# Kernel optimization log

Hardware: AMD Instinct MI355X
Metric: run time of the kernel (lower is better)

## Reference

```python
import jax, jax.numpy as jnp
import numpy as np

HIDDEN = 4096
NUM_HEADS = 32
NUM_KV_HEADS = 8
HEAD_DIM = 128


def setup_inputs() -> dict:
    key = jax.random.key(0)
    k0, k1, k2, k3, k4 = jax.random.split(key, 5)
    B, S = 1, 2048
    s = 0.02
    return {
        "hidden_states": jax.random.normal(k0, (B, S, HIDDEN), dtype=jnp.float32),
        "Wq": jax.random.normal(k1, (HIDDEN, NUM_HEADS * HEAD_DIM), dtype=jnp.float32) * s,
        "Wk": jax.random.normal(k2, (HIDDEN, NUM_KV_HEADS * HEAD_DIM), dtype=jnp.float32) * s,
        "Wv": jax.random.normal(k3, (HIDDEN, NUM_KV_HEADS * HEAD_DIM), dtype=jnp.float32) * s,
        "Wo": jax.random.normal(k4, (NUM_HEADS * HEAD_DIM, HIDDEN), dtype=jnp.float32) * s,
    }


def reference(hidden_states, Wq, Wk, Wv, Wo):
    B, S, _ = hidden_states.shape
    n_rep = NUM_HEADS // NUM_KV_HEADS
    # Projections -> [B, H, S, D]
    q = (hidden_states @ Wq).reshape(B, S, NUM_HEADS, HEAD_DIM).transpose(0, 2, 1, 3)
    k = (hidden_states @ Wk).reshape(B, S, NUM_KV_HEADS, HEAD_DIM).transpose(0, 2, 1, 3)
    v = (hidden_states @ Wv).reshape(B, S, NUM_KV_HEADS, HEAD_DIM).transpose(0, 2, 1, 3)
    # GQA expansion: repeat_interleave KV heads to match query head count
    k = jnp.repeat(k, n_rep, axis=1)
    v = jnp.repeat(v, n_rep, axis=1)
    scale = HEAD_DIM ** -0.5
    # Full [B, H, S, S] attention scores (faithful to the naive reference)
    scores = jnp.einsum("bhqd,bhkd->bhqk", q, k) * scale
    causal = jnp.tril(jnp.ones((S, S), dtype=bool))
    scores = jnp.where(causal[None, None], scores, jnp.float32(-jnp.inf))
    probs = jax.nn.softmax(scores, axis=-1)
    out = jnp.einsum("bhqk,bhkd->bhqd", probs, v)
    out = out.transpose(0, 2, 1, 3).reshape(B, S, NUM_HEADS * HEAD_DIM)
    return out @ Wo
```

## Files before the change

### kernel.cpp

```cpp
#include <hip/hip_runtime.h>
#include <hip/hip_bf16.h>

typedef __bf16 bf16;
typedef __bf16 bf16x4 __attribute__((ext_vector_type(4)));
typedef __bf16 bf16x8 __attribute__((ext_vector_type(8)));
typedef float  f32x4  __attribute__((ext_vector_type(4)));

#define SEQ  2048
#define HID  4096
#define QKVN 6144

__device__ __forceinline__ void gload_lds16(const void* g, void* l) {
  __builtin_amdgcn_global_load_lds(
      (const __attribute__((address_space(1))) void*)g,
      (__attribute__((address_space(3))) void*)l, 16, 0, 0);
}

__global__ __launch_bounds__(256) void cast_f32_bf16(const float* __restrict__ in,
                                                     bf16* __restrict__ out, int n) {
  int i = (blockIdx.x * 256 + threadIdx.x) * 4;
  int stride = gridDim.x * 256 * 4;
  for (; i < n; i += stride) {
    float4 v = *(const float4*)(in + i);
    bf16x4 o;
    o[0] = (bf16)v.x; o[1] = (bf16)v.y; o[2] = (bf16)v.z; o[3] = (bf16)v.w;
    *(bf16x4*)(out + i) = o;
  }
}

__global__ __launch_bounds__(256) void transpose_cast(const float* __restrict__ W,
                                                      bf16* __restrict__ Wt,
                                                      int N, int roff) {
  __shared__ float tile[32][33];
  int k0 = blockIdx.y * 32;
  int n0 = blockIdx.x * 32;
  int t = threadIdx.x;
  int r = t >> 5, c = t & 31;
#pragma unroll
  for (int p = 0; p < 4; ++p)
    tile[r + p * 8][c] = W[(size_t)(k0 + r + p * 8) * N + n0 + c];
  __syncthreads();
#pragma unroll
  for (int p = 0; p < 4; ++p)
    Wt[(size_t)(roff + n0 + r + p * 8) * 4096 + k0 + c] = (bf16)tile[c][r + p * 8];
}

__global__ __launch_bounds__(256) void transpose_v(const bf16* __restrict__ QKV,
                                                   bf16* __restrict__ Vt_g) {
  __shared__ bf16 tile[32][33];
  int s0 = blockIdx.x * 32;
  int d0 = blockIdx.y * 32;
  int g  = blockIdx.z;
  int t = threadIdx.x;
  int r = t >> 5, c = t & 31;
#pragma unroll
  for (int p = 0; p < 4; ++p)
    tile[r + p * 8][c] = QKV[(size_t)(s0 + r + p * 8) * QKVN + 5120 + g * 128 + d0 + c];
  __syncthreads();
#pragma unroll
  for (int p = 0; p < 4; ++p)
    Vt_g[(size_t)(g * 128 + d0 + r + p * 8) * SEQ + s0 + c] = tile[c][r + p * 8];
}

template <typename OUT_T>
__global__ __launch_bounds__(256) void gemm_bt(const bf16* __restrict__ A,
                                               const bf16* __restrict__ Bt,
                                               OUT_T* __restrict__ C,
                                               int K, int ldc) {
  __shared__ __align__(16) bf16 Abuf[128 * 64];
  __shared__ __align__(16) bf16 Bbuf[128 * 64];
  int m0 = blockIdx.y * 128, n0 = blockIdx.x * 128;
  int tid = threadIdx.x, w = tid >> 6, lane = tid & 63;
  int wr = w >> 1, wc = w & 1;
  int l15 = lane & 15, l4 = lane >> 4;
  f32x4 acc[4][4] = {};
  const int nk = K >> 6;
  for (int kt = 0; kt < nk; ++kt) {
    int k0 = kt << 6;
#pragma unroll
    for (int p = 0; p < 4; ++p) {
      int c = p * 256 + tid;
      int row = c >> 3, slot = c & 7;
      int ssl = (slot ^ (row & 7)) << 4;
      gload_lds16((const char*)(A + (size_t)(m0 + row) * K + k0) + ssl, (char*)Abuf + c * 16);
      gload_lds16((const char*)(Bt + (size_t)(n0 + row) * K + k0) + ssl, (char*)Bbuf + c * 16);
    }
    __syncthreads();
    bf16x8 af[4][2], bfr[4][2];
#pragma unroll
    for (int m = 0; m < 4; ++m)
#pragma unroll
      for (int kk = 0; kk < 2; ++kk) {
        int row = wr * 64 + m * 16 + l15;
        af[m][kk] = *(const bf16x8*)((const char*)Abuf + row * 128 +
                                     (((kk * 4 + l4) ^ (row & 7)) << 4));
      }
#pragma unroll
    for (int n = 0; n < 4; ++n)
#pragma unroll
      for (int kk = 0; kk < 2; ++kk) {
        int row = wc * 64 + n * 16 + l15;
        bfr[n][kk] = *(const bf16x8*)((const char*)Bbuf + row * 128 +
                                      (((kk * 4 + l4) ^ (row & 7)) << 4));
      }
#pragma unroll
    for (int kk = 0; kk < 2; ++kk)
#pragma unroll
      for (int m = 0; m < 4; ++m)
#pragma unroll
        for (int n = 0; n < 4; ++n)
          acc[m][n] = __builtin_amdgcn_mfma_f32_16x16x32_bf16(af[m][kk], bfr[n][kk],
                                                              acc[m][n], 0, 0, 0);
    __syncthreads();
  }
#pragma unroll
  for (int m = 0; m < 4; ++m)
#pragma unroll
    for (int n = 0; n < 4; ++n)
#pragma unroll
      for (int i = 0; i < 4; ++i) {
        int row = m0 + wr * 64 + m * 16 + l4 * 4 + i;
        int col = n0 + wc * 64 + n * 16 + l15;
        C[(size_t)row * ldc + col] = (OUT_T)acc[m][n][i];
      }
}

__global__ __launch_bounds__(512, 2) void attn_kernel(const bf16* __restrict__ QKV,
                                                      const bf16* __restrict__ Vt_g,
                                                      bf16* __restrict__ attn) {
  __shared__ __align__(16) bf16 Klds[2][64 * 128];
  __shared__ __align__(16) bf16 Vlds[2][64 * 128];
  __shared__ __align__(16) bf16 Plds[8 * 16 * 64];
  const int bid = blockIdx.x;
  const int g = bid & 7;
  const int rest = bid >> 3;
  const int hg = rest & 1;
  const int pair = rest >> 1;
  const int qb_a = pair, qb_b = 31 - pair;
  const int tid = threadIdx.x, w = tid >> 6, lane = tid & 63;
  const int hsel = w >> 2, qw = w & 3;
  const int h = g * 4 + hg * 2 + hsel;
  const int l15 = lane & 15, l4 = lane >> 4;
  const int wqA = qb_a * 64 + qw * 16;
  const int wqB = qb_b * 64 + qw * 16;
  const int qcol = h * 128;
  const int kcol = 4096 + g * 128;
  const float scale = 0.08838834764831845f;
  const float LOG2E = 1.4426950408889634f;

  const bf16* Vhead = Vt_g + (size_t)g * 128 * SEQ;

  bf16x8 aqA[4], aqB[4];
#pragma unroll
  for (int kc = 0; kc < 4; ++kc) {
    aqA[kc] = *(const bf16x8*)(QKV + (size_t)(wqA + l15) * QKVN + qcol + kc * 32 + l4 * 8);
    aqB[kc] = *(const bf16x8*)(QKV + (size_t)(wqB + l15) * QKVN + qcol + kc * 32 + l4 * 8);
  }

  f32x4 acc_oA[8] = {}, acc_oB[8] = {};
  float mA[4], lA[4], mB[4], lB[4];
#pragma unroll
  for (int i = 0; i < 4; ++i) { mA[i] = -1e30f; lA[i] = 0.f; mB[i] = -1e30f; lB[i] = 0.f; }

  auto stageKV = [&](int kb, int buf) {
#pragma unroll
    for (int j = 0; j < 2; ++j) {
      int c = tid + (j << 9);
      int krow = c >> 4, kslot = c & 15;
      gload_lds16((const char*)(QKV + (size_t)(kb + krow) * QKVN + kcol) +
                      ((kslot ^ (krow & 7)) << 4),
                  (char*)Klds[buf] + c * 16);
      int vrow = c >> 3, vslot = c & 7;
      gload_lds16(Vhead + (size_t)vrow * SEQ + kb + ((vslot ^ (vrow & 7)) << 3),
                  (char*)Vlds[buf] + c * 16);
    }
  };

  auto compute_block = [&](const bf16x8* aq, f32x4* acc_o, float* mrow, float* lrow,
                           int wq0, int kb, int cur) {
    const char* Kbuf = (const char*)Klds[cur];
    const char* Vbuf = (const char*)Vlds[cur];
    f32x4 accs[4] = {};
    __builtin_amdgcn_s_setprio(1);
#pragma unroll
    for (int n = 0; n < 4; ++n) {
      int row_ = n * 16 + l15;
      int sw = (row_ & 7) << 4;
#pragma unroll
      for (int kc = 0; kc < 4; ++kc) {
        bf16x8 bk = *(const bf16x8*)(Kbuf + row_ * 256 + ((kc * 64 + l4 * 16) ^ sw));
        accs[n] = __builtin_amdgcn_mfma_f32_16x16x32_bf16(aq[kc], bk, accs[n], 0, 0, 0);
      }
    }
    __builtin_amdgcn_s_setprio(0);
    bool needmask = (kb + 64 > wq0);
    float s[4][4];
#pragma unroll
    for (int n = 0; n < 4; ++n)
#pragma unroll
      for (int i = 0; i < 4; ++i) {
        float v = accs[n][i] * scale;
        if (needmask) {
          int ks = kb + n * 16 + l15;
          int qr = wq0 + l4 * 4 + i;
          if (ks > qr) v = -1e30f;
        }
        s[n][i] = v;
      }
    float t4[4];
#pragma unroll
    for (int i = 0; i < 4; ++i) {
      float t = fmaxf(fmaxf(s[0][i], s[1][i]), fmaxf(s[2][i], s[3][i]));
      t = fmaxf(t, __shfl_xor(t, 1));
      t = fmaxf(t, __shfl_xor(t, 2));
      t = fmaxf(t, __shfl_xor(t, 4));
      t = fmaxf(t, __shfl_xor(t, 8));
      t4[i] = t;
    }
    float dm = fmaxf(fmaxf(t4[0] - mrow[0], t4[1] - mrow[1]),
                     fmaxf(t4[2] - mrow[2], t4[3] - mrow[3]));
    if (!__all(dm <= 8.0f)) {
      float fac[4];
#pragma unroll
      for (int i = 0; i < 4; ++i) {
        float mnew = fmaxf(mrow[i], t4[i]);
        fac[i] = exp2f((mrow[i] - mnew) * LOG2E);
        mrow[i] = mnew;
        lrow[i] *= fac[i];
      }
#pragma unroll
      for (int n2 = 0; n2 < 8; ++n2)
#pragma unroll
        for (int i = 0; i < 4; ++i)
          acc_o[n2][i] *= fac[i];
    }
    float ps[4][4];
#pragma unroll
    for (int i = 0; i < 4; ++i) {
      float psum = 0.f;
#pragma unroll
      for (int n = 0; n < 4; ++n) {
        float p = exp2f((s[n][i] - mrow[i]) * LOG2E);
        ps[n][i] = p; psum += p;
      }
      psum += __shfl_xor(psum, 1);
      psum += __shfl_xor(psum, 2);
      psum += __shfl_xor(psum, 4);
      psum += __shfl_xor(psum, 8);
      lrow[i] += psum;
    }
    char* Pw = (char*)Plds + w * 2048;
#pragma unroll
    for (int n = 0; n < 4; ++n)
#pragma unroll
      for (int i = 0; i < 4; ++i) {
        int r = l4 * 4 + i;
        int b = (r * 128 + (n * 16 + l15) * 2) ^ ((r & 7) << 4);
        *(bf16*)(Pw + b) = (bf16)ps[n][i];
      }
    __builtin_amdgcn_sched_barrier(0);
    asm volatile("" ::: "memory");
    bf16x8 pa[2];
#pragma unroll
    for (int kc = 0; kc < 2; ++kc)
      pa[kc] = *(const bf16x8*)(Pw + (l15 * 128 + ((kc * 64 + l4 * 16) ^ ((l15 & 7) << 4))));
    __builtin_amdgcn_s_setprio(1);
#pragma unroll
    for (int n2 = 0; n2 < 8; ++n2) {
      int row_ = n2 * 16 + l15;
      int sw = (row_ & 7) << 4;
#pragma unroll
      for (int kc = 0; kc < 2; ++kc) {
        bf16x8 bv = *(const bf16x8*)(Vbuf + row_ * 128 + ((kc * 64 + l4 * 16) ^ sw));
        acc_o[n2] = __builtin_amdgcn_mfma_f32_16x16x32_bf16(pa[kc], bv, acc_o[n2], 0, 0, 0);
      }
    }
    __builtin_amdgcn_s_setprio(0);
    asm volatile("" ::: "memory");
  };

  stageKV(0, 0);
  __syncthreads();

  int cur = 0;
  for (int kbi = 0; kbi <= qb_b; ++kbi) {
    int kb = kbi * 64;
    if (kbi < qb_b) stageKV(kb + 64, cur ^ 1);
    if (kbi <= qb_a) compute_block(aqA, acc_oA, mA, lA, wqA, kb, cur);
    compute_block(aqB, acc_oB, mB, lB, wqB, kb, cur);
    __syncthreads();
    cur ^= 1;
  }

#pragma unroll
  for (int n2 = 0; n2 < 8; ++n2)
#pragma unroll
    for (int i = 0; i < 4; ++i) {
      int col = qcol + n2 * 16 + l15;
      attn[(size_t)(wqA + l4 * 4 + i) * 4096 + col] = (bf16)(acc_oA[n2][i] / lA[i]);
      attn[(size_t)(wqB + l4 * 4 + i) * 4096 + col] = (bf16)(acc_oB[n2][i] / lB[i]);
    }
}

extern "C" void kernel_launch(void* const* d_in, const int* in_sizes, int n_in,
                              void* d_out, int out_size, void* d_ws, size_t ws_size,
                              hipStream_t stream) {
  const float* X  = (const float*)d_in[0];
  const float* Wq = (const float*)d_in[1];
  const float* Wk = (const float*)d_in[2];
  const float* Wv = (const float*)d_in[3];
  const float* Wo = (const float*)d_in[4];
  float* out = (float*)d_out;

  const size_t XB_OFF  = 0;
  const size_t WT_OFF  = 16777216;
  const size_t VT_OFF  = WT_OFF + 33554432;
  const size_t QKV_OFF = 16777216 + 50331648;
  if (ws_size < (size_t)92274688) return;

  char* ws = (char*)d_ws;
  bf16* Xb    = (bf16*)(ws + XB_OFF);
  bf16* Wt    = (bf16*)(ws + WT_OFF);
  bf16* Vt_g  = (bf16*)(ws + VT_OFF);
  bf16* QKV   = (bf16*)(ws + QKV_OFF);
  bf16* attnb = Xb;

  cast_f32_bf16<<<2048, 256, 0, stream>>>(X, Xb, SEQ * HID);
  transpose_cast<<<dim3(4096 / 32, 4096 / 32), 256, 0, stream>>>(Wq, Wt, 4096, 0);
  transpose_cast<<<dim3(1024 / 32, 4096 / 32), 256, 0, stream>>>(Wk, Wt, 1024, 4096);
  transpose_cast<<<dim3(1024 / 32, 4096 / 32), 256, 0, stream>>>(Wv, Wt, 1024, 5120);
  gemm_bt<bf16><<<dim3(QKVN / 128, SEQ / 128), 256, 0, stream>>>(Xb, Wt, QKV, HID, QKVN);
  transpose_cast<<<dim3(4096 / 32, 4096 / 32), 256, 0, stream>>>(Wo, Wt, 4096, 0);
  transpose_v<<<dim3(SEQ / 32, 4, 8), 256, 0, stream>>>(QKV, Vt_g);
  attn_kernel<<<256, 512, 0, stream>>>(QKV, Vt_g, attnb);
  gemm_bt<float><<<dim3(4096 / 128, SEQ / 128), 256, 0, stream>>>(attnb, Wt, out, HID, 4096);
}
```

Measured before the change: 379.0 us.

## Interleave QK and PV MFMAs for both query tiles sharing K/V LDS loads

Restructures the attention inner step so the two query tiles (A and B) are processed together. Each K and V fragment read from LDS now feeds two MFMAs instead of one, which halves LDS reads and gives the scheduler independent MFMA chains to interleave. Softmax is split into its own helper. Because this doubles live accumulators and registers, the launch bound drops to one block per SIMD group, reducing occupancy in exchange for more ILP and fewer LDS reads.

```diff
diff --git a/kernel.cpp b/kernel.cpp
--- a/kernel.cpp
+++ b/kernel.cpp
@@ -125,7 +125,7 @@
       }
 }
 
-__global__ __launch_bounds__(512, 2) void attn_kernel(const bf16* __restrict__ QKV,
+__global__ __launch_bounds__(512, 1) void attn_kernel(const bf16* __restrict__ QKV,
                                                       const bf16* __restrict__ Vt_g,
                                                       bf16* __restrict__ attn) {
   __shared__ __align__(16) bf16 Klds[2][64 * 128];
@@ -176,23 +176,8 @@
     }
   };
 
-  auto compute_block = [&](const bf16x8* aq, f32x4* acc_o, float* mrow, float* lrow,
-                           int wq0, int kb, int cur) {
-    const char* Kbuf = (const char*)Klds[cur];
-    const char* Vbuf = (const char*)Vlds[cur];
-    f32x4 accs[4] = {};
-    __builtin_amdgcn_s_setprio(1);
-#pragma unroll
-    for (int n = 0; n < 4; ++n) {
-      int row_ = n * 16 + l15;
-      int sw = (row_ & 7) << 4;
-#pragma unroll
-      for (int kc = 0; kc < 4; ++kc) {
-        bf16x8 bk = *(const bf16x8*)(Kbuf + row_ * 256 + ((kc * 64 + l4 * 16) ^ sw));
-        accs[n] = __builtin_amdgcn_mfma_f32_16x16x32_bf16(aq[kc], bk, accs[n], 0, 0, 0);
-      }
-    }
-    __builtin_amdgcn_s_setprio(0);
+  auto softmax_and_P = [&](f32x4* accs, float* mrow, float* lrow, f32x4* acc_o,
+                           int wq0, int kb, bf16x8* pa) {
     bool needmask = (kb + 64 > wq0);
     float s[4][4];
 #pragma unroll
@@ -260,19 +245,69 @@
       }
     __builtin_amdgcn_sched_barrier(0);
     asm volatile("" ::: "memory");
-    bf16x8 pa[2];
 #pragma unroll
     for (int kc = 0; kc < 2; ++kc)
       pa[kc] = *(const bf16x8*)(Pw + (l15 * 128 + ((kc * 64 + l4 * 16) ^ ((l15 & 7) << 4))));
+    __builtin_amdgcn_sched_barrier(0);
+    asm volatile("" ::: "memory");
+  };
+
+  auto compute_tile = [&](int kb, int cur, bool doA) {
+    const char* Kbuf = (const char*)Klds[cur];
+    const char* Vbuf = (const char*)Vlds[cur];
+    f32x4 accsA[4] = {}, accsB[4] = {};
     __builtin_amdgcn_s_setprio(1);
-#pragma unroll
-    for (int n2 = 0; n2 < 8; ++n2) {
-      int row_ = n2 * 16 + l15;
-      int sw = (row_ & 7) << 4;
-#pragma unroll
-      for (int kc = 0; kc < 2; ++kc) {
-        bf16x8 bv = *(const bf16x8*)(Vbuf + row_ * 128 + ((kc * 64 + l4 * 16) ^ sw));
-        acc_o[n2] = __builtin_amdgcn_mfma_f32_16x16x32_bf16(pa[kc], bv, acc_o[n2], 0, 0, 0);
+    if (doA) {
+#pragma unroll
+      for (int n = 0; n < 4; ++n) {
+        int row_ = n * 16 + l15;
+        int sw = (row_ & 7) << 4;
+#pragma unroll
+        for (int kc = 0; kc < 4; ++kc) {
+          bf16x8 bk = *(const bf16x8*)(Kbuf + row_ * 256 + ((kc * 64 + l4 * 16) ^ sw));
+          accsA[n] = __builtin_amdgcn_mfma_f32_16x16x32_bf16(aqA[kc], bk, accsA[n], 0, 0, 0);
+          accsB[n] = __builtin_amdgcn_mfma_f32_16x16x32_bf16(aqB[kc], bk, accsB[n], 0, 0, 0);
+        }
+      }
+    } else {
+#pragma unroll
+      for (int n = 0; n < 4; ++n) {
+        int row_ = n * 16 + l15;
+        int sw = (row_ & 7) << 4;
+#pragma unroll
+        for (int kc = 0; kc < 4; ++kc) {
+          bf16x8 bk = *(const bf16x8*)(Kbuf + row_ * 256 + ((kc * 64 + l4 * 16) ^ sw));
+          accsB[n] = __builtin_amdgcn_mfma_f32_16x16x32_bf16(aqB[kc], bk, accsB[n], 0, 0, 0);
+        }
+      }
+    }
+    __builtin_amdgcn_s_setprio(0);
+    bf16x8 paA[2], paB[2];
+    if (doA) softmax_and_P(accsA, mA, lA, acc_oA, wqA, kb, paA);
+    softmax_and_P(accsB, mB, lB, acc_oB, wqB, kb, paB);
+    __builtin_amdgcn_s_setprio(1);
+    if (doA) {
+#pragma unroll
+      for (int n2 = 0; n2 < 8; ++n2) {
+        int row_ = n2 * 16 + l15;
+        int sw = (row_ & 7) << 4;
+#pragma unroll
+        for (int kc = 0; kc < 2; ++kc) {
+          bf16x8 bv = *(const bf16x8*)(Vbuf + row_ * 128 + ((kc * 64 + l4 * 16) ^ sw));
+          acc_oA[n2] = __builtin_amdgcn_mfma_f32_16x16x32_bf16(paA[kc], bv, acc_oA[n2], 0, 0, 0);
+          acc_oB[n2] = __builtin_amdgcn_mfma_f32_16x16x32_bf16(paB[kc], bv, acc_oB[n2], 0, 0, 0);
+        }
+      }
+    } else {
+#pragma unroll
+      for (int n2 = 0; n2 < 8; ++n2) {
+        int row_ = n2 * 16 + l15;
+        int sw = (row_ & 7) << 4;
+#pragma unroll
+        for (int kc = 0; kc < 2; ++kc) {
+          bf16x8 bv = *(const bf16x8*)(Vbuf + row_ * 128 + ((kc * 64 + l4 * 16) ^ sw));
+          acc_oB[n2] = __builtin_amdgcn_mfma_f32_16x16x32_bf16(paB[kc], bv, acc_oB[n2], 0, 0, 0);
+        }
       }
     }
     __builtin_amdgcn_s_setprio(0);
@@ -286,8 +321,7 @@
   for (int kbi = 0; kbi <= qb_b; ++kbi) {
     int kb = kbi * 64;
     if (kbi < qb_b) stageKV(kb + 64, cur ^ 1);
-    if (kbi <= qb_a) compute_block(aqA, acc_oA, mA, lA, wqA, kb, cur);
-    compute_block(aqB, acc_oB, mB, lB, wqB, kb, cur);
+    compute_tile(kb, cur, kbi <= qb_a);
     __syncthreads();
     cur ^= 1;
   }
```

Result: slower. 390.3 us (+3.0%).
